# Kernel optimization log

Measured on AMD Instinct MI355X. Metric: run time of the kernel, lower is better.

## Reference

```python
import jax, jax.numpy as jnp
import numpy as np

B, S, D, H = 2, 2048, 1024, 16
DK = D // H
NEG = -65504.0  # matches torch masked_fill value in source


def setup_inputs() -> dict:
    key = jax.random.key(0)
    ks = jax.random.split(key, 5)
    scale = 1.0 / np.sqrt(D)
    return {
        "x": jax.random.normal(ks[0], (B, S, D), dtype=jnp.float32),
        "W_q": jax.random.normal(ks[1], (D, D), dtype=jnp.float32) * scale,
        "W_k": jax.random.normal(ks[2], (D, D), dtype=jnp.float32) * scale,
        "W_v": jax.random.normal(ks[3], (D, D), dtype=jnp.float32) * scale,
        "W_o": jax.random.normal(ks[4], (D, D), dtype=jnp.float32) * scale,
    }


def reference(x, W_q, W_k, W_v, W_o):
    b, s, d = x.shape
    # nn.Linear(x) = x @ W.T ; split heads -> [b, h, s, dk]
    def proj(W):
        return (x @ W.T).reshape(b, s, H, DK).transpose(0, 2, 1, 3)
    q, k, v = proj(W_q), proj(W_k), proj(W_v)
    scores = jnp.einsum("bhqd,bhkd->bhqk", q, k) / jnp.sqrt(jnp.float32(DK))
    causal = jnp.tril(jnp.ones((s, s), dtype=bool))  # True where attending allowed
    scores = jnp.where(causal, scores, NEG)
    attn = jax.nn.softmax(scores, axis=-1)  # attn_pdrop=0 -> dropout is identity
    out = jnp.einsum("bhqk,bhkd->bhqd", attn, v)
    out = out.transpose(0, 2, 1, 3).reshape(b, s, d)
    return out @ W_o.T
```

## Files before the change

### kernel.cpp

```cpp
#include <hip/hip_runtime.h>
#include <hip/hip_bf16.h>

typedef __attribute__((ext_vector_type(4))) float f32x4;
typedef __attribute__((ext_vector_type(8))) short bf16x8;

#define Bn 2
#define Sn 2048
#define Dn 1024
#define Hn 16
#define DKn 64
#define Mrows (Bn * Sn)

__device__ __forceinline__ unsigned short f2bf(float f) {
  unsigned int x = __float_as_uint(f);
  x += 0x7fffu + ((x >> 16) & 1u);
  return (unsigned short)(x >> 16);
}

__device__ __forceinline__ float bf2f(unsigned short u) {
  return __uint_as_float(((unsigned int)u) << 16);
}

__device__ __forceinline__ unsigned int cvtpk(float lo, float hi) {
  unsigned int r;
  asm("v_cvt_pk_bf16_f32 %0, %1, %2" : "=v"(r) : "v"(lo), "v"(hi));
  return r;
}

__device__ __forceinline__ f32x4 mfma16(bf16x8 a, bf16x8 b, f32x4 c) {
  return __builtin_amdgcn_mfma_f32_16x16x32_bf16(a, b, c, 0, 0, 0);
}

__device__ __forceinline__ void gload_lds16(const unsigned short* g, unsigned short* l) {
  __builtin_amdgcn_global_load_lds(
      (const __attribute__((address_space(1))) void*)g,
      (__attribute__((address_space(3))) void*)l, 16, 0, 0);
}

__global__ __launch_bounds__(256)
void cvt_all(const float* __restrict__ x,  const float* __restrict__ wq,
             const float* __restrict__ wk, const float* __restrict__ wv,
             const float* __restrict__ wo,
             unsigned short* __restrict__ xb,  unsigned short* __restrict__ wqb,
             unsigned short* __restrict__ wkb, unsigned short* __restrict__ wvb,
             unsigned short* __restrict__ wob) {
  int i = (blockIdx.x * 256 + threadIdx.x) * 4;
  const float* src; unsigned short* dst; int off;
  int r = i >> 20;
  if (r < 4)       { src = x;  dst = xb;  off = i; }
  else if (r == 4) { src = wq; dst = wqb; off = i & 1048575; }
  else if (r == 5) { src = wk; dst = wkb; off = i & 1048575; }
  else if (r == 6) { src = wv; dst = wvb; off = i & 1048575; }
  else             { src = wo; dst = wob; off = i & 1048575; }
  float4 v = *(const float4*)(src + off);
  ushort4 o;
  o.x = f2bf(v.x); o.y = f2bf(v.y); o.z = f2bf(v.z); o.w = f2bf(v.w);
  *(ushort4*)(dst + off) = o;
}

template<int MODE>
__device__ __forceinline__ void gemm_body(const unsigned short* __restrict__ A,
                                          const unsigned short* __restrict__ W,
                                          unsigned short* __restrict__ Cb,
                                          float* __restrict__ Cf,
                                          unsigned short* As,
                                          unsigned short* Bs) {
  const int K = Dn, N = Dn;
  const int tid  = threadIdx.x;
  const int wid  = tid >> 6;
  const int lane = tid & 63;
  const int l15  = lane & 15;
  const int lg   = lane >> 4;
  const int row0 = blockIdx.x * 128;
  const int col0 = blockIdx.y * 128;
  const int wr = (wid >> 1) * 64;
  const int wc = (wid & 1) * 64;

  f32x4 acc[4][4] = {};

  const int lrow  = lane >> 3;
  const int sgran = (lane & 7) ^ lrow;
  const int swz   = l15 & 7;

  for (int kt = 0; kt < K; kt += 64) {
#pragma unroll
    for (int p = 0; p < 4; ++p) {
      int chunk = p * 4 + wid;
      int r = chunk * 8 + lrow;
      gload_lds16(A + (size_t)(row0 + r) * K + kt + sgran * 8, &As[chunk * 512]);
    }
#pragma unroll
    for (int p = 0; p < 4; ++p) {
      int chunk = p * 4 + wid;
      int r = chunk * 8 + lrow;
      gload_lds16(W + (size_t)(col0 + r) * K + kt + sgran * 8, &Bs[chunk * 512]);
    }
    __syncthreads();

#pragma unroll
    for (int kk = 0; kk < 2; ++kk) {
      bf16x8 af[4], bfr[4];
#pragma unroll
      for (int m = 0; m < 4; ++m)
        af[m] = *(const bf16x8*)(&As[(wr + m * 16 + l15) * 64 +
                                     (((kk * 4 + lg) ^ swz) * 8)]);
#pragma unroll
      for (int n = 0; n < 4; ++n)
        bfr[n] = *(const bf16x8*)(&Bs[(wc + n * 16 + l15) * 64 +
                                      (((kk * 4 + lg) ^ swz) * 8)]);
#pragma unroll
      for (int m = 0; m < 4; ++m)
#pragma unroll
        for (int n = 0; n < 4; ++n)
          acc[m][n] = mfma16(af[m], bfr[n], acc[m][n]);
    }
    __syncthreads();
  }

#pragma unroll
  for (int m = 0; m < 4; ++m)
#pragma unroll
    for (int n = 0; n < 4; ++n) {
      int r0 = row0 + wr + m * 16 + lg * 4;
      int c  = col0 + wc + n * 16 + l15;
      if (MODE == 2) {
        int b = r0 >> 11, s = r0 & 2047;
        int h = c >> 6,  d = c & 63;
        ushort4 pw;
        pw.x = f2bf(acc[m][n][0]); pw.y = f2bf(acc[m][n][1]);
        pw.z = f2bf(acc[m][n][2]); pw.w = f2bf(acc[m][n][3]);
        *(ushort4*)(Cb + ((((size_t)b * Hn + h) * DKn + d) << 11) + s) = pw;
      } else {
#pragma unroll
        for (int j = 0; j < 4; ++j) {
          size_t idx = (size_t)(r0 + j) * N + c;
          float v = acc[m][n][j];
          if (MODE == 3)      Cf[idx] = v;
          else if (MODE == 0) Cb[idx] = f2bf(v * 0.125f);
          else                Cb[idx] = f2bf(v);
        }
      }
    }
}

__global__ __launch_bounds__(256)
void gemm_qkv(const unsigned short* __restrict__ A,
              const unsigned short* __restrict__ W0,
              const unsigned short* __restrict__ W1,
              const unsigned short* __restrict__ W2,
              unsigned short* __restrict__ C0,
              unsigned short* __restrict__ C1,
              unsigned short* __restrict__ C2) {
  __shared__ unsigned short As[128 * 64];
  __shared__ unsigned short Bs[128 * 64];
  if (blockIdx.z == 0)      gemm_body<0>(A, W0, C0, nullptr, As, Bs);
  else if (blockIdx.z == 1) gemm_body<1>(A, W1, C1, nullptr, As, Bs);
  else                      gemm_body<2>(A, W2, C2, nullptr, As, Bs);
}

__global__ __launch_bounds__(256)
void gemm_out(const unsigned short* __restrict__ A,
              const unsigned short* __restrict__ W,
              float* __restrict__ C) {
  __shared__ unsigned short As[128 * 64];
  __shared__ unsigned short Bs[128 * 64];
  gemm_body<3>(A, W, nullptr, C, As, Bs);
}

__global__ __launch_bounds__(256)
void attn_part(const unsigned short* __restrict__ Qg,
               const unsigned short* __restrict__ Kg,
               const unsigned short* __restrict__ Vtg,
               unsigned short* __restrict__ Og,
               unsigned short* __restrict__ Pb,
               float* __restrict__ Pml) {
  const int bid = blockIdx.x;
  const int bh = bid & 31;
  const int j  = bid >> 5;
  const int bb = bh >> 4, hh = bh & 15;
  const int tid = threadIdx.x, wid = tid >> 6, lane = tid & 63;
  const int l15 = lane & 15, lg = lane >> 4;
  const int wq = wid * 32;
  const size_t baseQ = (size_t)bb * Sn * Dn + (size_t)hh * DKn;
  const size_t baseV = (size_t)bh * DKn * Sn;

  __shared__ unsigned short Ks[2][64 * 64];
  __shared__ unsigned short Vts[2][64 * 64];
  __shared__ unsigned short Ps[4][32 * 72];

  const int lrow  = lane >> 3;
  const int sgran = (lane & 7) ^ lrow;
  const int swz   = l15 & 7;

  const int g0 = 17 * j;
  int qt = 0;
  while ((qt + 1) * (qt + 2) <= g0) ++qt;
  int kt = g0 - qt * (qt + 1);

  int sqt = qt, skt = kt;
  auto stage = [&](int t, int b) {
    const int k0 = t << 6;
#pragma unroll
    for (int p = 0; p < 2; ++p) {
      int c = p * 4 + wid;
      int r = c * 8 + lrow;
      gload_lds16(Kg + baseQ + (size_t)(k0 + r) * Dn + sgran * 8, &Ks[b][c * 512]);
    }
#pragma unroll
    for (int p = 0; p < 2; ++p) {
      int c = p * 4 + wid;
      int dr = c * 8 + lrow;
      gload_lds16(Vtg + baseV + (size_t)dr * Sn + k0 + sgran * 8, &Vts[b][c * 512]);
    }
  };
  auto advs = [&]() { ++skt; if (skt == 2 * sqt + 2) { skt = 0; ++sqt; } };

  stage(skt, 0); advs();
  __syncthreads();

  bf16x8 qf[2][2];
  auto loadQ = [&](int qtile) {
    const int q0 = qtile * 128;
#pragma unroll
    for (int qm = 0; qm < 2; ++qm)
#pragma unroll
      for (int kd = 0; kd < 2; ++kd)
        qf[qm][kd] = *(const bf16x8*)(Qg + baseQ +
                     (size_t)(q0 + wq + qm * 16 + l15) * Dn + kd * 32 + lg * 8);
  };
  loadQ(qt);

  f32x4 oacc[2][4] = {};
  float mrun[2] = {-1e30f, -1e30f};
  float lrun[2] = {0.f, 0.f};
  int pstart = kt;

  for (int i = 0; i < 17; ++i) {
    const int cur = i & 1;
    if (i < 16) { stage(skt, cur ^ 1); advs(); }
    const int k0 = kt << 6;
    const int q0 = qt * 128;

    if (k0 <= q0 + wq + 31) {
      f32x4 sf[2][4] = {};
      __builtin_amdgcn_s_setprio(1);
#pragma unroll
      for (int kn = 0; kn < 4; ++kn)
#pragma unroll
        for (int kd = 0; kd < 2; ++kd) {
          bf16x8 kf = *(const bf16x8*)(&Ks[cur][(kn * 16 + l15) * 64 +
                                              (((kd * 4 + lg) ^ swz) * 8)]);
          sf[0][kn] = mfma16(kf, qf[0][kd], sf[0][kn]);
          sf[1][kn] = mfma16(kf, qf[1][kd], sf[1][kn]);
        }
      __builtin_amdgcn_s_setprio(0);

      if (k0 + 63 > q0 + wq) {
#pragma unroll
        for (int qm = 0; qm < 2; ++qm) {
          int qq = q0 + wq + qm * 16 + l15;
#pragma unroll
          for (int kn = 0; kn < 4; ++kn)
#pragma unroll
            for (int jj = 0; jj < 4; ++jj) {
              int key = k0 + kn * 16 + lg * 4 + jj;
              if (key > qq) sf[qm][kn][jj] = -1e30f;
            }
        }
      }

#pragma unroll
      for (int qm = 0; qm < 2; ++qm) {
        float t = sf[qm][0][0];
#pragma unroll
        for (int kn = 0; kn < 4; ++kn)
#pragma unroll
          for (int jj = 0; jj < 4; ++jj) t = fmaxf(t, sf[qm][kn][jj]);
        t = fmaxf(t, __shfl_xor(t, 16));
        t = fmaxf(t, __shfl_xor(t, 32));
        if (__any(t > mrun[qm] + 8.0f)) {
          float mnew = fmaxf(mrun[qm], t);
          float corr = __expf(mrun[qm] - mnew);
          mrun[qm] = mnew;
          lrun[qm] *= corr;
#pragma unroll
          for (int dn = 0; dn < 4; ++dn) oacc[qm][dn] *= corr;
        }
        const float m = mrun[qm];
        float rs = 0.f;
#pragma unroll
        for (int kn = 0; kn < 4; ++kn) {
#pragma unroll
          for (int jj = 0; jj < 4; ++jj) {
            float p = __expf(sf[qm][kn][jj] - m);
            sf[qm][kn][jj] = p;
            rs += p;
          }
          uint2 pw;
          pw.x = cvtpk(sf[qm][kn][0], sf[qm][kn][1]);
          pw.y = cvtpk(sf[qm][kn][2], sf[qm][kn][3]);
          *(uint2*)(&Ps[wid][(qm * 16 + l15) * 72 + kn * 16 + lg * 4]) = pw;
        }
        rs += __shfl_xor(rs, 16);
        rs += __shfl_xor(rs, 32);
        lrun[qm] += rs;
      }

      __builtin_amdgcn_s_setprio(1);
#pragma unroll
      for (int kk = 0; kk < 2; ++kk) {
        bf16x8 pf[2];
#pragma unroll
        for (int qm = 0; qm < 2; ++qm)
          pf[qm] = *(const bf16x8*)(&Ps[wid][(qm * 16 + l15) * 72 + kk * 32 + lg * 8]);
#pragma unroll
        for (int dn = 0; dn < 4; ++dn) {
          bf16x8 vf = *(const bf16x8*)(&Vts[cur][(dn * 16 + l15) * 64 +
                                               (((kk * 4 + lg) ^ swz) * 8)]);
#pragma unroll
          for (int qm = 0; qm < 2; ++qm)
            oacc[qm][dn] = mfma16(vf, pf[qm], oacc[qm][dn]);
        }
      }
      __builtin_amdgcn_s_setprio(0);
    }

    const bool segend = (kt == 2 * qt + 1);
    if (segend || i == 16) {
      if (pstart == 0 && segend) {
#pragma unroll
        for (int qm = 0; qm < 2; ++qm) {
          float rinv = 1.0f / lrun[qm];
          int row = q0 + wq + qm * 16 + l15;
#pragma unroll
          for (int dn = 0; dn < 4; ++dn) {
            ushort4 ow;
            ow.x = f2bf(oacc[qm][dn][0] * rinv);
            ow.y = f2bf(oacc[qm][dn][1] * rinv);
            ow.z = f2bf(oacc[qm][dn][2] * rinv);
            ow.w = f2bf(oacc[qm][dn][3] * rinv);
            *(ushort4*)(Og + baseQ + (size_t)row * Dn + dn * 16 + lg * 4) = ow;
          }
        }
      } else {
        const int seg_s = qt * (qt + 1);
        const int ord = pstart ? ((seg_s + pstart) / 17 - seg_s / 17) : 0;
        const size_t slot = (size_t)((bh * 16 + qt) * 3 + ord);
#pragma unroll
        for (int qm = 0; qm < 2; ++qm) {
          int rl = wq + qm * 16 + l15;
#pragma unroll
          for (int dn = 0; dn < 4; ++dn) {
            ushort4 ow;
            ow.x = f2bf(oacc[qm][dn][0]);
            ow.y = f2bf(oacc[qm][dn][1]);
            ow.z = f2bf(oacc[qm][dn][2]);
            ow.w = f2bf(oacc[qm][dn][3]);
            *(ushort4*)(Pb + slot * 8192 + (size_t)rl * 64 + dn * 16 + lg * 4) = ow;
          }
          if (lg == 0) {
            Pml[slot * 256 + rl] = mrun[qm];
            Pml[slot * 256 + 128 + rl] = lrun[qm];
          }
        }
      }
      if (i < 16) {
        ++qt; kt = 0; pstart = 0;
        loadQ(qt);
#pragma unroll
        for (int qm = 0; qm < 2; ++qm) {
          mrun[qm] = -1e30f; lrun[qm] = 0.f;
#pragma unroll
          for (int dn = 0; dn < 4; ++dn) oacc[qm][dn] = f32x4{0.f, 0.f, 0.f, 0.f};
        }
      }
    } else {
      ++kt;
    }
    __syncthreads();
  }
}

__global__ __launch_bounds__(256)
void attn_combine(const unsigned short* __restrict__ Pb,
                  const float* __restrict__ Pml,
                  unsigned short* __restrict__ Og) {
  const int b = blockIdx.x;
  const int bh = b >> 4, qt = b & 15;
  const int seg_s = qt * (qt + 1);
  const int seg_e = seg_s + 2 * qt + 2;
  const int c0 = (seg_s / 17 + 1) * 17;
  if (c0 >= seg_e) return;
  const int np = (c0 + 17 < seg_e) ? 3 : 2;
  const int bb = bh >> 4, hh = bh & 15;
  const size_t baseQ = (size_t)bb * Sn * Dn + (size_t)hh * DKn;
  const int q0 = qt * 128;
  const int slot0 = b * 3;
  const int r = threadIdx.x >> 1;
  const int c32 = (threadIdx.x & 1) * 32;

  float m0 = Pml[(size_t)slot0 * 256 + r];
  float l0 = Pml[(size_t)slot0 * 256 + 128 + r];
  float m1 = Pml[(size_t)(slot0 + 1) * 256 + r];
  float l1 = Pml[(size_t)(slot0 + 1) * 256 + 128 + r];
  float m2 = -1e30f, l2 = 0.f;
  if (np == 3) {
    m2 = Pml[(size_t)(slot0 + 2) * 256 + r];
    l2 = Pml[(size_t)(slot0 + 2) * 256 + 128 + r];
  }
  float M = fmaxf(fmaxf(m0, m1), m2);
  float w0 = __expf(m0 - M), w1 = __expf(m1 - M);
  float w2 = (np == 3) ? __expf(m2 - M) : 0.f;
  float L = l0 * w0 + l1 * w1 + l2 * w2;

  float acc[32];
#pragma unroll
  for (int k = 0; k < 32; ++k) acc[k] = 0.f;

  auto accum = [&](int p, float w) {
    const unsigned short* src = Pb + (size_t)(slot0 + p) * 8192 + (size_t)r * 64 + c32;
#pragma unroll
    for (int k4 = 0; k4 < 8; ++k4) {
      ushort4 v = *(const ushort4*)(src + k4 * 4);
      acc[k4 * 4 + 0] += w * bf2f(v.x);
      acc[k4 * 4 + 1] += w * bf2f(v.y);
      acc[k4 * 4 + 2] += w * bf2f(v.z);
      acc[k4 * 4 + 3] += w * bf2f(v.w);
    }
  };
  accum(0, w0);
  accum(1, w1);
  if (np == 3) accum(2, w2);

  float rinv = 1.0f / L;
#pragma unroll
  for (int k4 = 0; k4 < 8; ++k4) {
    ushort4 o;
    o.x = f2bf(acc[k4 * 4 + 0] * rinv);
    o.y = f2bf(acc[k4 * 4 + 1] * rinv);
    o.z = f2bf(acc[k4 * 4 + 2] * rinv);
    o.w = f2bf(acc[k4 * 4 + 3] * rinv);
    *(ushort4*)(Og + baseQ + (size_t)(q0 + r) * Dn + c32 + k4 * 4) = o;
  }
}

extern "C" void kernel_launch(void* const* d_in, const int* in_sizes, int n_in,
                              void* d_out, int out_size, void* d_ws, size_t ws_size,
                              hipStream_t stream) {
  const float* x  = (const float*)d_in[0];
  const float* Wq = (const float*)d_in[1];
  const float* Wk = (const float*)d_in[2];
  const float* Wv = (const float*)d_in[3];
  const float* Wo = (const float*)d_in[4];
  float* out = (float*)d_out;

  char* ws = (char*)d_ws;
  size_t off = 0;
  unsigned short* xb  = (unsigned short*)(ws + off); off += (size_t)Mrows * Dn * 2;
  unsigned short* wqb = (unsigned short*)(ws + off); off += (size_t)Dn * Dn * 2;
  unsigned short* wkb = (unsigned short*)(ws + off); off += (size_t)Dn * Dn * 2;
  unsigned short* wvb = (unsigned short*)(ws + off); off += (size_t)Dn * Dn * 2;
  unsigned short* wob = (unsigned short*)(ws + off); off += (size_t)Dn * Dn * 2;
  unsigned short* Qb  = (unsigned short*)(ws + off); off += (size_t)Mrows * Dn * 2;
  unsigned short* Kb  = (unsigned short*)(ws + off); off += (size_t)Mrows * Dn * 2;
  unsigned short* Vtb = (unsigned short*)(ws + off); off += (size_t)Mrows * Dn * 2;
  unsigned short* Ob  = (unsigned short*)(ws + off); off += (size_t)Mrows * Dn * 2;
  unsigned short* Pb  = (unsigned short*)(ws + off); off += (size_t)512 * 3 * 8192 * 2;
  float*          Pml = (float*)(ws + off);          off += (size_t)512 * 3 * 256 * 4;

  cvt_all<<<8192, 256, 0, stream>>>(x, Wq, Wk, Wv, Wo, xb, wqb, wkb, wvb, wob);
  gemm_qkv<<<dim3(Mrows / 128, Dn / 128, 3), 256, 0, stream>>>(xb, wqb, wkb, wvb, Qb, Kb, Vtb);
  attn_part<<<512, 256, 0, stream>>>(Qb, Kb, Vtb, Ob, Pb, Pml);
  attn_combine<<<512, 256, 0, stream>>>(Pb, Pml, Ob);
  gemm_out<<<dim3(Mrows / 128, Dn / 128), 256, 0, stream>>>(Ob, wob, out);
}
```

Measured before the change: 126.5 us.

## Double-buffer GEMM LDS tiles to overlap global loads with MFMA

Restructures the shared GEMM body used by the QKV and output projections into a two-stage pipeline. The LDS buffers for A and W are doubled so the next K-tile's direct global-to-LDS loads are issued while the current tile is multiplied, with explicit vmcnt waits and barriers replacing the single-buffer load/sync/compute loop. It also raises wave priority around the MFMA block via s_setprio. The cost targeted is exposed global-load latency in each K iteration. In exchange LDS use per block doubles to 64 KB, which may lower occupancy, and the hand-written vmcnt counts assume a fixed number of outstanding loads per stage.

```diff
diff --git a/kernel.cpp b/kernel.cpp
--- a/kernel.cpp
+++ b/kernel.cpp
@@ -82,40 +82,65 @@
   const int sgran = (lane & 7) ^ lrow;
   const int swz   = l15 & 7;
 
-  for (int kt = 0; kt < K; kt += 64) {
+  auto stage = [&](int kt, int b) {
 #pragma unroll
     for (int p = 0; p < 4; ++p) {
       int chunk = p * 4 + wid;
       int r = chunk * 8 + lrow;
-      gload_lds16(A + (size_t)(row0 + r) * K + kt + sgran * 8, &As[chunk * 512]);
+      gload_lds16(A + (size_t)(row0 + r) * K + kt + sgran * 8,
+                  &As[b * 8192 + chunk * 512]);
     }
 #pragma unroll
     for (int p = 0; p < 4; ++p) {
       int chunk = p * 4 + wid;
       int r = chunk * 8 + lrow;
-      gload_lds16(W + (size_t)(col0 + r) * K + kt + sgran * 8, &Bs[chunk * 512]);
-    }
-    __syncthreads();
-
+      gload_lds16(W + (size_t)(col0 + r) * K + kt + sgran * 8,
+                  &Bs[b * 8192 + chunk * 512]);
+    }
+  };
+
+  auto compute = [&](int b) {
 #pragma unroll
     for (int kk = 0; kk < 2; ++kk) {
       bf16x8 af[4], bfr[4];
 #pragma unroll
       for (int m = 0; m < 4; ++m)
-        af[m] = *(const bf16x8*)(&As[(wr + m * 16 + l15) * 64 +
+        af[m] = *(const bf16x8*)(&As[b * 8192 + (wr + m * 16 + l15) * 64 +
                                      (((kk * 4 + lg) ^ swz) * 8)]);
 #pragma unroll
       for (int n = 0; n < 4; ++n)
-        bfr[n] = *(const bf16x8*)(&Bs[(wc + n * 16 + l15) * 64 +
+        bfr[n] = *(const bf16x8*)(&Bs[b * 8192 + (wc + n * 16 + l15) * 64 +
                                       (((kk * 4 + lg) ^ swz) * 8)]);
+      __builtin_amdgcn_s_setprio(1);
 #pragma unroll
       for (int m = 0; m < 4; ++m)
 #pragma unroll
         for (int n = 0; n < 4; ++n)
           acc[m][n] = mfma16(af[m], bfr[n], acc[m][n]);
-    }
-    __syncthreads();
+      __builtin_amdgcn_s_setprio(0);
+    }
+  };
+
+  stage(0, 0);
+  stage(64, 1);
+#pragma unroll 1
+  for (int kt = 0; kt < 14; ++kt) {
+    asm volatile("s_waitcnt vmcnt(8)" ::: "memory");
+    __builtin_amdgcn_sched_barrier(0);
+    __builtin_amdgcn_s_barrier();
+    compute(kt & 1);
+    __builtin_amdgcn_sched_barrier(0);
+    __builtin_amdgcn_s_barrier();
+    stage((kt + 2) * 64, kt & 1);
   }
+  asm volatile("s_waitcnt vmcnt(8)" ::: "memory");
+  __builtin_amdgcn_sched_barrier(0);
+  __builtin_amdgcn_s_barrier();
+  compute(0);
+  asm volatile("s_waitcnt vmcnt(0)" ::: "memory");
+  __builtin_amdgcn_sched_barrier(0);
+  __builtin_amdgcn_s_barrier();
+  compute(1);
 
 #pragma unroll
   for (int m = 0; m < 4; ++m)
@@ -151,8 +176,8 @@
               unsigned short* __restrict__ C0,
               unsigned short* __restrict__ C1,
               unsigned short* __restrict__ C2) {
-  __shared__ unsigned short As[128 * 64];
-  __shared__ unsigned short Bs[128 * 64];
+  __shared__ unsigned short As[2 * 128 * 64];
+  __shared__ unsigned short Bs[2 * 128 * 64];
   if (blockIdx.z == 0)      gemm_body<0>(A, W0, C0, nullptr, As, Bs);
   else if (blockIdx.z == 1) gemm_body<1>(A, W1, C1, nullptr, As, Bs);
   else                      gemm_body<2>(A, W2, C2, nullptr, As, Bs);
@@ -162,8 +187,8 @@
 void gemm_out(const unsigned short* __restrict__ A,
               const unsigned short* __restrict__ W,
               float* __restrict__ C) {
-  __shared__ unsigned short As[128 * 64];
-  __shared__ unsigned short Bs[128 * 64];
+  __shared__ unsigned short As[2 * 128 * 64];
+  __shared__ unsigned short Bs[2 * 128 * 64];
   gemm_body<3>(A, W, nullptr, C, As, Bs);
 }
 
```

Result: faster. 118.2 us (-6.6%).
